# Kernel tuning notes

Measured on AMD Instinct MI355X. Metric: run time of the kernel, lower is better.

## Reference

```python
import jax, jax.numpy as jnp
import numpy as np

B, N, C = 1, 2048, 1024
H, D = 16, 64          # num_heads, head_dim
S = 8                  # number of frames; tokens per frame = N // S
NEG_INF = jnp.float32(-1e30)  # stand-in for -inf, numerically safe under jit


def setup_inputs() -> dict:
    key = jax.random.key(0)
    ks = jax.random.split(key, 8)
    x = jax.random.normal(ks[0], (B, N, C), dtype=jnp.float32)
    # tokens grouped contiguously by frame (sorted frame ids)
    frame_ids = jnp.repeat(jnp.arange(S, dtype=jnp.int32), N // S)
    is_hub = jax.random.bernoulli(ks[1], 0.05, (N,))
    adj = jax.random.bernoulli(ks[2], 0.25, (S, S))
    adj = adj.at[jnp.arange(S), jnp.arange(S)].set(True)  # frames always see self
    frame_bias = jax.random.normal(ks[3], (S, S), dtype=jnp.float32) * 0.1
    Wqkv = jax.random.normal(ks[4], (C, 3 * C), dtype=jnp.float32) * 0.02
    bqkv = jnp.zeros((3 * C,), dtype=jnp.float32)
    Wproj = jax.random.normal(ks[5], (C, C), dtype=jnp.float32) * 0.02
    bproj = jnp.zeros((C,), dtype=jnp.float32)
    return {"x": x, "frame_ids": frame_ids, "is_hub": is_hub, "adj": adj,
            "frame_bias": frame_bias, "Wqkv": Wqkv, "bqkv": bqkv,
            "Wproj": Wproj, "bproj": bproj}


def reference(x, frame_ids, is_hub, adj, frame_bias, Wqkv, bqkv, Wproj, bproj):
    # qkv projection: (B,N,3C) -> (3,B,H,N,D)
    qkv = (x @ Wqkv + bqkv).reshape(B, N, 3, H, D).transpose(2, 0, 3, 1, 4)
    q, k, v = qkv[0], qkv[1], qkv[2]

    # flex_attention: scores scaled by 1/sqrt(D) BEFORE score_mod
    scores = jnp.einsum("bhnd,bhmd->bhnm", q, k) * (D ** -0.5)

    # score_mod, vectorized over all (qi,kj) pairs:
    fi = frame_ids                                   # (N,)
    allow = adj[fi][:, fi]                           # (N,N) frame adjacency per token pair
    diff_frame = fi[:, None] != fi[None, :]
    hub_block = diff_frame & (is_hub[:, None] | is_hub[None, :])
    allow = allow & ~hub_block                       # mask_hub_tokens=True
    bias = frame_bias[fi][:, fi]                     # soft_mask=True: add frame-level bias

    scores = jnp.where(allow, scores + bias, NEG_INF)  # broadcast over (b,h)
    attn = jax.nn.softmax(scores, axis=-1)
    out = jnp.einsum("bhnm,bhmd->bhnd", attn, v)
    out = out.transpose(0, 2, 1, 3).reshape(B, N, C)
    return out @ Wproj + bproj
```

## Files before the change

kernel.cpp:

```cpp
#include <hip/hip_runtime.h>

#define NTOK 2048
#define CDIM 1024
#define NHEAD 16
#define HDIM 64
#define NFRM 8
#define FTOK 256

typedef unsigned short ushort;
typedef unsigned long long u64;
typedef __attribute__((ext_vector_type(8))) short short8;
typedef __attribute__((ext_vector_type(8))) ushort ushort8;
typedef __attribute__((ext_vector_type(4))) ushort ushort4v;
typedef __attribute__((ext_vector_type(4))) float floatx4;

__device__ __forceinline__ ushort f2bf(float f) {
    unsigned int u = __float_as_uint(f);
    return (ushort)((u + 0x7fffu + ((u >> 16) & 1u)) >> 16);
}

__device__ __forceinline__ void gload_lds16(const void* g, void* l) {
    __builtin_amdgcn_global_load_lds(
        (const __attribute__((address_space(1))) unsigned int*)(uintptr_t)g,
        (__attribute__((address_space(3))) unsigned int*)(unsigned int)(uintptr_t)l,
        16, 0, 0);
}

__global__ __launch_bounds__(256)
void prep_kernel(const float* __restrict__ x, ushort* __restrict__ xb,
                 const float* __restrict__ Wqkv, ushort* __restrict__ wqkvT,
                 const float* __restrict__ Wproj, ushort* __restrict__ wprojT,
                 const int* __restrict__ is_hub, u64* __restrict__ hubmask)
{
    __shared__ ushort LT[64][72];
    const int b = blockIdx.x, t = threadIdx.x;

    if (b < 2048) {
        int i = b * 256 + t;
        float4 f = ((const float4*)x)[i];
        ushort4v o = { f2bf(f.x), f2bf(f.y), f2bf(f.z), f2bf(f.w) };
        ((ushort4v*)xb)[i] = o;
        return;
    }
    if (b >= 3072) {
        if (t < NTOK / 64) {
            u64 m = 0;
            for (int j = 0; j < 64; ++j)
                m |= (u64)(is_hub[t * 64 + j] != 0) << j;
            hubmask[t] = m;
        }
        return;
    }

    const float* W; ushort* WT; int K, N, n0, k0;
    if (b < 2816) { int idx = b - 2048; W = Wqkv;  WT = wqkvT;  K = 1024; N = 3072;
                    n0 = (idx % 48) * 64; k0 = (idx / 48) * 64; }
    else          { int idx = b - 2816; W = Wproj; WT = wprojT; K = 1024; N = 1024;
                    n0 = (idx & 15) * 64; k0 = (idx >> 4) * 64; }

    const int kr = t >> 4, nc = t & 15;
#pragma unroll
    for (int i = 0; i < 4; ++i) {
        int k = kr + i * 16;
        float4 w4 = *(const float4*)(W + (size_t)(k0 + k) * N + n0 + nc * 4);
        LT[nc*4+0][k] = f2bf(w4.x);
        LT[nc*4+1][k] = f2bf(w4.y);
        LT[nc*4+2][k] = f2bf(w4.z);
        LT[nc*4+3][k] = f2bf(w4.w);
    }
    __syncthreads();
    const int n = t >> 2;
#pragma unroll
    for (int half = 0; half < 2; ++half) {
        int kc = (t & 3) + 4 * half;
        ushort8 v = *(const ushort8*)&LT[n][kc * 8];
        *(ushort8*)(WT + (size_t)(n0 + n) * K + k0 + kc * 8) = v;
    }
}

template<int BM>
__global__ __launch_bounds__(256)
void gemm_bt_kernel(const ushort* __restrict__ A, const ushort* __restrict__ BT,
                    const float* __restrict__ bias, void* __restrict__ out,
                    ushort* __restrict__ vtb,
                    int M, int N, int K, int mode)
{
    constexpr int MI = BM / 32;
    __shared__ ushort As[2][BM * 32];
    __shared__ ushort Bs[2][128 * 32];

    const int t = threadIdx.x;
    const int wave = t >> 6, lane = t & 63;
    const int quad = lane >> 4, l15 = lane & 15;
    const int row0 = blockIdx.y * BM, col0 = blockIdx.x * 128;
    const int wm = (wave >> 1) * (BM / 2), wn = (wave & 1) * 64;

    const int sr = lane >> 2;
    const int sc = (lane & 3) * 8;
    const int ra = wave * (BM / 4);
    const int rb = wave * 32;

    floatx4 acc[MI][4];
#pragma unroll
    for (int i = 0; i < MI; ++i)
#pragma unroll
        for (int j = 0; j < 4; ++j) acc[i][j] = (floatx4){0.f, 0.f, 0.f, 0.f};

#pragma unroll
    for (int ii = 0; ii < BM / 64; ++ii)
        gload_lds16(A + (size_t)(row0 + ra + ii * 16 + sr) * K + sc, &As[0][(ra + ii * 16) * 32]);
    gload_lds16(BT + (size_t)(col0 + rb      + sr) * K + sc, &Bs[0][ rb       * 32]);
    gload_lds16(BT + (size_t)(col0 + rb + 16 + sr) * K + sc, &Bs[0][(rb + 16) * 32]);

    const int nk = K >> 5;
    for (int ki = 0; ki < nk; ++ki) {
        __syncthreads();
        if (ki + 1 < nk) {
            const int kn = (ki + 1) << 5;
            const int b = (ki + 1) & 1;
#pragma unroll
            for (int ii = 0; ii < BM / 64; ++ii)
                gload_lds16(A + (size_t)(row0 + ra + ii * 16 + sr) * K + kn + sc, &As[b][(ra + ii * 16) * 32]);
            gload_lds16(BT + (size_t)(col0 + rb      + sr) * K + kn + sc, &Bs[b][ rb       * 32]);
            gload_lds16(BT + (size_t)(col0 + rb + 16 + sr) * K + kn + sc, &Bs[b][(rb + 16) * 32]);
        }
        const ushort* as = As[ki & 1];
        const ushort* bs = Bs[ki & 1];

        short8 af[MI], bfr[4];
#pragma unroll
        for (int i = 0; i < MI; ++i)
            af[i] = *(const short8*)&as[(wm + i * 16 + l15) * 32 + quad * 8];
#pragma unroll
        for (int j = 0; j < 4; ++j)
            bfr[j] = *(const short8*)&bs[(wn + j * 16 + l15) * 32 + quad * 8];
#pragma unroll
        for (int i = 0; i < MI; ++i)
#pragma unroll
            for (int j = 0; j < 4; ++j)
                acc[i][j] = __builtin_amdgcn_mfma_f32_16x16x32_bf16(af[i], bfr[j], acc[i][j], 0, 0, 0);
    }

    if (mode == 0) {
        float* outf = (float*)out;
#pragma unroll
        for (int j = 0; j < 4; ++j) {
            int col = col0 + wn + j * 16 + l15;
            float bb = bias[col];
#pragma unroll
            for (int i = 0; i < MI; ++i) {
                int rowb = row0 + wm + i * 16 + quad * 4;
#pragma unroll
                for (int r = 0; r < 4; ++r)
                    outf[(size_t)(rowb + r) * N + col] = acc[i][j][r] + bb;
            }
        }
    } else {
        ushort* outb = (ushort*)out;
#pragma unroll
        for (int j = 0; j < 4; ++j) {
            int col = col0 + wn + j * 16 + l15;
            float bb = bias[col];
            int part = col >> 10, hh = (col >> 6) & 15, d = col & 63;
            if (part < 2) {
                int half = d >> 5, qk = (d & 31) >> 3, elem = d & 7;
                ushort* base = outb + (size_t)(part * NHEAD + hh) * (NTOK * HDIM);
#pragma unroll
                for (int i = 0; i < MI; ++i) {
                    int rowb = row0 + wm + i * 16 + quad * 4;
#pragma unroll
                    for (int r = 0; r < 4; ++r) {
                        int tok = rowb + r;
                        int tile = tok >> 6, kk = tok & 63;
                        int nt = kk >> 4, lk = kk & 15;
                        base[(size_t)tile * 4096 + ((nt * 2 + half) * 64 + qk * 16 + lk) * 8 + elem]
                            = f2bf(acc[i][j][r] + bb);
                    }
                }
            } else {
                int dt = d >> 4, lv = d & 15;
                ushort* base = vtb + (size_t)hh * (NTOK * HDIM);
#pragma unroll
                for (int i = 0; i < MI; ++i) {
                    int rowb = row0 + wm + i * 16 + quad * 4;
                    int tile = rowb >> 6, kk = rowb & 63;
                    int half = kk >> 5, qv = (kk & 31) >> 3, elem = kk & 7;
                    ushort4v pk = { f2bf(acc[i][j][0] + bb), f2bf(acc[i][j][1] + bb),
                                    f2bf(acc[i][j][2] + bb), f2bf(acc[i][j][3] + bb) };
                    *(ushort4v*)&base[(size_t)tile * 4096 + ((dt * 2 + half) * 64 + qv * 16 + lv) * 8 + elem] = pk;
                }
            }
        }
    }
}

__global__ __launch_bounds__(512, 4)
void attn_tile_kernel(const ushort* __restrict__ qkvb,
                      const ushort* __restrict__ vTb,
                      const int* __restrict__ frame_ids,
                      const u64* __restrict__ hubmask,
                      const int* __restrict__ adj,
                      const float* __restrict__ frame_bias,
                      ushort* __restrict__ attnb)
{
    __shared__ ushort Ps[8][16 * 72];
    __shared__ float  Om[4][64][21];

    const int t = threadIdx.x;
    const int wave = t >> 6, lane = t & 63;
    const int wq = wave & 3, wk = wave >> 2;
    const int quad = lane >> 4, l15 = lane & 15;
    const int b = blockIdx.x;
    const int h = b & 15, q0 = (b >> 4) * 64;

    const ushort* Qh = qkvb + (size_t)h * (NTOK * HDIM);
    const ushort* Kh = qkvb + (size_t)(NHEAD + h) * (NTOK * HDIM);
    const ushort* Vh = vTb + (size_t)h * (NTOK * HDIM);

    const ushort* qt = Qh + (size_t)(q0 >> 6) * 4096;
    short8 aq0 = *(const short8*)(qt + ((wq * 2 + 0) * 64 + lane) * 8);
    short8 aq1 = *(const short8*)(qt + ((wq * 2 + 1) * 64 + lane) * 8);

    const int fq = frame_ids[q0];
    unsigned vpack = 0; int nv = 0;
#pragma unroll
    for (int f = 0; f < NFRM; ++f)
        if (adj[fq * NFRM + f]) { vpack |= (unsigned)f << (3 * nv); ++nv; }

    const u64 hmq = hubmask[q0 >> 6];
    int qh[4];
#pragma unroll
    for (int r = 0; r < 4; ++r) qh[r] = (int)((hmq >> (wq * 16 + quad * 4 + r)) & 1);

    float lpart[4] = {0.f, 0.f, 0.f, 0.f};
    floatx4 oacc[4];
#pragma unroll
    for (int dt = 0; dt < 4; ++dt) oacc[dt] = (floatx4){0.f, 0.f, 0.f, 0.f};

    const float C1 = 0.18033688011112042f;
    const float L2E = 1.4426950408889634f;

    const int nmine = nv * 2;
    int vt = wk;
    for (int j = 0; j < nmine; ++j, vt += 2) {
        const int fj = (int)((vpack >> (3 * (vt >> 2))) & 7u);
        const int k0 = fj * FTOK + (vt & 3) * 64;
        const float fbl = frame_bias[fq * NFRM + fj] * L2E;
        const bool same = (fj == fq);
        const u64 hmk = hubmask[k0 >> 6];

        const ushort* kt = Kh + (size_t)(k0 >> 6) * 4096;
        const ushort* vtp = Vh + (size_t)(k0 >> 6) * 4096;
        short8 kf[8], vf[8];
#pragma unroll
        for (int idx = 0; idx < 8; ++idx)
            kf[idx] = *(const short8*)(kt + (idx * 64 + lane) * 8);
#pragma unroll
        for (int idx = 0; idx < 8; ++idx)
            vf[idx] = *(const short8*)(vtp + (idx * 64 + lane) * 8);

        floatx4 s[4];
#pragma unroll
        for (int nt = 0; nt < 4; ++nt) {
            s[nt] = (floatx4){0.f, 0.f, 0.f, 0.f};
            s[nt] = __builtin_amdgcn_mfma_f32_16x16x32_bf16(aq0, kf[2*nt],     s[nt], 0, 0, 0);
            s[nt] = __builtin_amdgcn_mfma_f32_16x16x32_bf16(aq1, kf[2*nt + 1], s[nt], 0, 0, 0);
        }

        float mkf[4];
#pragma unroll
        for (int nt = 0; nt < 4; ++nt) {
            int kb = (int)(((unsigned)(hmk >> (nt * 16)) >> l15) & 1u);
            mkf[nt] = (same || !kb) ? 1.f : 0.f;
        }
        float mrf[4];
#pragma unroll
        for (int r = 0; r < 4; ++r) mrf[r] = (same || !qh[r]) ? 1.f : 0.f;

#pragma unroll
        for (int r = 0; r < 4; ++r) {
            float ps = 0.f;
            ushort* prow = &Ps[wave][(quad * 4 + r) * 72 + l15];
#pragma unroll
            for (int nt = 0; nt < 4; ++nt) {
                float e = __builtin_amdgcn_exp2f(fmaf(s[nt][r], C1, fbl));
                float p = e * mkf[nt] * mrf[r];
                ps += p;
                prow[nt * 16] = f2bf(p);
            }
            lpart[r] += ps;
        }

        short8 ap0 = *(const short8*)&Ps[wave][l15 * 72 + quad * 8];
        short8 ap1 = *(const short8*)&Ps[wave][l15 * 72 + 32 + quad * 8];
#pragma unroll
        for (int dt = 0; dt < 4; ++dt) {
            oacc[dt] = __builtin_amdgcn_mfma_f32_16x16x32_bf16(ap0, vf[2*dt],     oacc[dt], 0, 0, 0);
            oacc[dt] = __builtin_amdgcn_mfma_f32_16x16x32_bf16(ap1, vf[2*dt + 1], oacc[dt], 0, 0, 0);
        }
    }

    if (wk == 1) {
#pragma unroll
        for (int dt = 0; dt < 4; ++dt)
#pragma unroll
            for (int r = 0; r < 4; ++r) Om[wq][lane][dt * 4 + r] = oacc[dt][r];
#pragma unroll
        for (int r = 0; r < 4; ++r) Om[wq][lane][16 + r] = lpart[r];
    }
    __syncthreads();
    if (wk == 1) return;

#pragma unroll
    for (int dt = 0; dt < 4; ++dt)
#pragma unroll
        for (int r = 0; r < 4; ++r) oacc[dt][r] += Om[wq][lane][dt * 4 + r];
#pragma unroll
    for (int r = 0; r < 4; ++r) lpart[r] += Om[wq][lane][16 + r];

    float linv[4];
#pragma unroll
    for (int r = 0; r < 4; ++r) {
        float ls = lpart[r];
        ls += __shfl_xor(ls, 1);
        ls += __shfl_xor(ls, 2);
        ls += __shfl_xor(ls, 4);
        ls += __shfl_xor(ls, 8);
        linv[r] = 1.0f / ls;
    }

#pragma unroll
    for (int dt = 0; dt < 4; ++dt) {
        int col = h * HDIM + dt * 16 + l15;
#pragma unroll
        for (int r = 0; r < 4; ++r) {
            int row = q0 + wq * 16 + quad * 4 + r;
            attnb[(size_t)row * CDIM + col] = f2bf(oacc[dt][r] * linv[r]);
        }
    }
}

extern "C" void kernel_launch(void* const* d_in, const int* in_sizes, int n_in,
                              void* d_out, int out_size, void* d_ws, size_t ws_size,
                              hipStream_t stream)
{
    const float* x          = (const float*)d_in[0];
    const int*   frame_ids  = (const int*)d_in[1];
    const int*   is_hub     = (const int*)d_in[2];
    const int*   adj        = (const int*)d_in[3];
    const float* frame_bias = (const float*)d_in[4];
    const float* Wqkv       = (const float*)d_in[5];
    const float* bqkv       = (const float*)d_in[6];
    const float* Wproj      = (const float*)d_in[7];
    const float* bproj      = (const float*)d_in[8];
    float* out = (float*)d_out;

    ushort* xb     = (ushort*)d_ws;
    ushort* wqkvT  = xb     + 2097152;
    ushort* wprojT = wqkvT  + 3145728;
    ushort* qkvb   = wprojT + 1048576;
    ushort* vTb    = qkvb   + 6291456;
    ushort* attnb  = vTb    + 2097152;
    u64*    hubmask = (u64*)(attnb + 2097152);

    prep_kernel<<<dim3(3073), dim3(256), 0, stream>>>(
        x, xb, Wqkv, wqkvT, Wproj, wprojT, is_hub, hubmask);

    gemm_bt_kernel<128><<<dim3(3 * CDIM / 128, NTOK / 128), dim3(256), 0, stream>>>(
        xb, wqkvT, bqkv, qkvb, vTb, NTOK, 3 * CDIM, CDIM, 1);

    attn_tile_kernel<<<dim3(512), dim3(512), 0, stream>>>(
        qkvb, vTb, frame_ids, hubmask, adj, frame_bias, attnb);

    gemm_bt_kernel<64><<<dim3(CDIM / 128, NTOK / 64), dim3(256), 0, stream>>>(
        attnb, wprojT, bproj, out, nullptr, NTOK, CDIM, CDIM, 0);
}
```

Measured before the change: 142.7 us.

## Pack P row stores with cvt_pk_bf16, permute V layout, raise MFMA priority

The P tile is now written to LDS as one packed 8-byte store per row, using the hardware v_cvt_pk_bf16_f32 instruction instead of four scalar bf16 stores with software rounding. To keep the P·V product correct with this permuted key order, the V-transpose writer in the projection kernel permutes its key slots to match, at the cost of turning its vector store into scalar stores. It also wraps the MFMA blocks in s_setprio to favour matrix issue across waves. The hardware conversion may round slightly differently from the software routine.

```diff
diff --git a/kernel.cpp b/kernel.cpp
--- a/kernel.cpp
+++ b/kernel.cpp
@@ -17,6 +17,12 @@
 __device__ __forceinline__ ushort f2bf(float f) {
     unsigned int u = __float_as_uint(f);
     return (ushort)((u + 0x7fffu + ((u >> 16) & 1u)) >> 16);
+}
+
+__device__ __forceinline__ unsigned int cvt_pk_bf16(float lo, float hi) {
+    unsigned int r;
+    asm volatile("v_cvt_pk_bf16_f32 %0, %1, %2" : "=v"(r) : "v"(lo), "v"(hi));
+    return r;
 }
 
 __device__ __forceinline__ void gload_lds16(const void* g, void* l) {
@@ -184,10 +190,13 @@
                 for (int i = 0; i < MI; ++i) {
                     int rowb = row0 + wm + i * 16 + quad * 4;
                     int tile = rowb >> 6, kk = rowb & 63;
-                    int half = kk >> 5, qv = (kk & 31) >> 3, elem = kk & 7;
-                    ushort4v pk = { f2bf(acc[i][j][0] + bb), f2bf(acc[i][j][1] + bb),
-                                    f2bf(acc[i][j][2] + bb), f2bf(acc[i][j][3] + bb) };
-                    *(ushort4v*)&base[(size_t)tile * 4096 + ((dt * 2 + half) * 64 + qv * 16 + lv) * 8 + elem] = pk;
+                    int bslot = ((kk & 15) << 2) | (kk >> 4);
+#pragma unroll
+                    for (int r = 0; r < 4; ++r) {
+                        int s = bslot + 4 * r;
+                        int off = ((dt * 2 + (s >> 5)) * 64 + ((s >> 3) & 3) * 16 + lv) * 8 + (s & 7);
+                        base[(size_t)tile * 4096 + off] = f2bf(acc[i][j][r] + bb);
+                    }
                 }
             }
         }
@@ -261,11 +270,15 @@
 
         floatx4 s[4];
 #pragma unroll
+        for (int nt = 0; nt < 4; ++nt)
+            s[nt] = (floatx4){0.f, 0.f, 0.f, 0.f};
+        __builtin_amdgcn_s_setprio(1);
+#pragma unroll
         for (int nt = 0; nt < 4; ++nt) {
-            s[nt] = (floatx4){0.f, 0.f, 0.f, 0.f};
             s[nt] = __builtin_amdgcn_mfma_f32_16x16x32_bf16(aq0, kf[2*nt],     s[nt], 0, 0, 0);
             s[nt] = __builtin_amdgcn_mfma_f32_16x16x32_bf16(aq1, kf[2*nt + 1], s[nt], 0, 0, 0);
         }
+        __builtin_amdgcn_s_setprio(0);
 
         float mkf[4];
 #pragma unroll
@@ -279,25 +292,28 @@
 
 #pragma unroll
         for (int r = 0; r < 4; ++r) {
-            float ps = 0.f;
-            ushort* prow = &Ps[wave][(quad * 4 + r) * 72 + l15];
+            float pv[4];
 #pragma unroll
             for (int nt = 0; nt < 4; ++nt) {
                 float e = __builtin_amdgcn_exp2f(fmaf(s[nt][r], C1, fbl));
-                float p = e * mkf[nt] * mrf[r];
-                ps += p;
-                prow[nt * 16] = f2bf(p);
+                pv[nt] = e * mkf[nt] * mrf[r];
             }
-            lpart[r] += ps;
+            lpart[r] += (pv[0] + pv[1]) + (pv[2] + pv[3]);
+            uint2 pk;
+            pk.x = cvt_pk_bf16(pv[0], pv[1]);
+            pk.y = cvt_pk_bf16(pv[2], pv[3]);
+            *(uint2*)&Ps[wave][(quad * 4 + r) * 72 + l15 * 4] = pk;
         }
 
         short8 ap0 = *(const short8*)&Ps[wave][l15 * 72 + quad * 8];
         short8 ap1 = *(const short8*)&Ps[wave][l15 * 72 + 32 + quad * 8];
+        __builtin_amdgcn_s_setprio(1);
 #pragma unroll
         for (int dt = 0; dt < 4; ++dt) {
             oacc[dt] = __builtin_amdgcn_mfma_f32_16x16x32_bf16(ap0, vf[2*dt],     oacc[dt], 0, 0, 0);
             oacc[dt] = __builtin_amdgcn_mfma_f32_16x16x32_bf16(ap1, vf[2*dt + 1], oacc[dt], 0, 0, 0);
         }
+        __builtin_amdgcn_s_setprio(0);
     }
 
     if (wk == 1) {
```

Result: no change. 141.9 us (-0.6%).
